# Kernel optimization log

Measured on AMD Instinct MI355X. Metric: run time of the kernel, lower is better.

Reference implementation:

```python
import jax, jax.numpy as jnp
import numpy as np

PC_RANGE = (-51.2, -51.2, -5.0, 51.2, 51.2, 3.0)
E, CAMS, LVLS = 256, 6, 4
LVL_HW = [(64, 176), (32, 88), (16, 44), (8, 22)]


def setup_inputs() -> dict:
    key = jax.random.key(0)
    ks = jax.random.split(key, 16)
    B, N = 2, 6400
    inp = {
        'instance_feature': jax.random.normal(ks[0], (B, N, E), jnp.float32),
        'anchor': jax.random.normal(ks[1], (B, N, 11), jnp.float32),
        'projection': jax.random.uniform(ks[2], (B, CAMS, 4, 4), jnp.float32),
    }
    for i, (H, W) in enumerate(LVL_HW):
        inp[f'feat{i}'] = jax.random.normal(ks[3 + i], (B, CAMS, E, H, W), jnp.float32)
    # learned params (random, not the zero-init of the module, to exercise the math)
    inp['attn_w'] = jax.random.normal(ks[8], (CAMS * LVLS, E), jnp.float32) * 0.02
    inp['attn_b'] = jax.random.normal(ks[9], (CAMS * LVLS,), jnp.float32) * 0.02
    inp['vp_w'] = jax.random.normal(ks[10], (E, E), jnp.float32) * (1.0 / np.sqrt(E))
    inp['vp_b'] = jnp.zeros((E,), jnp.float32)
    inp['op_w'] = jax.random.normal(ks[11], (E, E), jnp.float32) * (1.0 / np.sqrt(E))
    inp['op_b'] = jnp.zeros((E,), jnp.float32)
    return inp


def _bilinear_sample(feat, x, y):
    """feat: [BN, C, H, W]; x, y: [BN, N] pixel coords.
    Bilinear, zeros padding, align_corners=True (pixel coords == uv directly).
    Returns [BN, N, C]."""
    BN, C, H, W = feat.shape
    x0 = jnp.floor(x); y0 = jnp.floor(y)
    wx1 = x - x0; wx0 = 1.0 - wx1
    wy1 = y - y0; wy0 = 1.0 - wy1
    feat_flat = feat.reshape(BN, C, H * W)
    b = jnp.arange(BN)[:, None]

    def corner(xi, yi, w):
        valid = (xi >= 0) & (xi <= W - 1) & (yi >= 0) & (yi <= H - 1)
        xi_c = jnp.clip(xi, 0, W - 1).astype(jnp.int32)
        yi_c = jnp.clip(yi, 0, H - 1).astype(jnp.int32)
        idx = yi_c * W + xi_c                      # [BN, N]
        v = feat_flat[b, :, idx]                   # [BN, N, C]
        return v * (w * valid.astype(w.dtype))[..., None]

    return (corner(x0, y0, wx0 * wy0) + corner(x0 + 1, y0, wx1 * wy0)
            + corner(x0, y0 + 1, wx0 * wy1) + corner(x0 + 1, y0 + 1, wx1 * wy1))


def reference(instance_feature, anchor, projection, feat0, feat1, feat2, feat3,
              attn_w, attn_b, vp_w, vp_b, op_w, op_b):
    B, N, _ = instance_feature.shape
    feats = [feat0, feat1, feat2, feat3]
    # attention weights over cams x levels (softmax over levels, dim=-1)
    attn = (instance_feature @ attn_w.T + attn_b).reshape(B, N, CAMS, LVLS)
    attn = jax.nn.softmax(attn, axis=-1)
    # anchor center -> world coords
    xyz = jax.nn.sigmoid(anchor[..., :3])
    pr = jnp.asarray(PC_RANGE, dtype=anchor.dtype)
    xyz_world = xyz * (pr[3:6] - pr[0:3]) + pr[0:3]
    xyz_h = jnp.concatenate([xyz_world, jnp.ones((B, N, 1), anchor.dtype)], axis=-1)
    xyz_cam = jnp.einsum('bcij,bnj->bcni', projection, xyz_h)   # [B,CAMS,N,4]
    depth = jnp.maximum(xyz_cam[..., 2:3], 1e-4)
    uv = xyz_cam[..., :2] / depth                               # [B,CAMS,N,2] pixel coords
    BN = B * CAMS
    x = uv[..., 0].reshape(BN, N)
    y = uv[..., 1].reshape(BN, N)
    sampled = []
    for feat in feats:
        H, W = feat.shape[-2], feat.shape[-1]
        s = _bilinear_sample(feat.reshape(BN, E, H, W), x, y)   # [BN,N,E]
        sampled.append(s.reshape(B, CAMS, N, E))
    S = jnp.stack(sampled, axis=0)                              # [L,B,CAMS,N,E]
    out = jnp.einsum('lbcne,bncl->bne', S, attn)
    out = out @ vp_w.T + vp_b
    out = (out + instance_feature) @ op_w.T + op_b
    return out
```

## Files before the change

kernel.cpp:

```cpp
#include <hip/hip_runtime.h>
#include <hip/hip_fp16.h>
#include <math.h>

#define B_ 2
#define N_ 6400
#define E_ 256
#define C_ 6
#define L_ 4
#define SL2_ 128

__device__ __host__ constexpr int HWH[4] = {64, 32, 16, 8};
__device__ __host__ constexpr int HWW[4] = {176, 88, 44, 22};
__device__ __host__ constexpr int LOFF[4] = {0, 11264, 14080, 14784};
#define HWT 14960

struct __align__(8) H4 { __half2 lo, hi; };

typedef __attribute__((ext_vector_type(8))) _Float16 half8;
typedef __attribute__((ext_vector_type(4))) _Float16 half4;
typedef __attribute__((ext_vector_type(4))) float floatx4;

__global__ __launch_bounds__(256) void prep_kernel(
    const float* __restrict__ inst, const float* __restrict__ anchor,
    const float* __restrict__ proj, const float* __restrict__ attn_w,
    const float* __restrict__ attn_b,
    uint4* __restrict__ meta_w, int4* __restrict__ meta_b)
{
    __shared__ float AWT[256 * 24];
    __shared__ float ts[256 * 33];

    const int tid = threadIdx.x;

    for (int idx = tid; idx < 24 * 256; idx += 256) {
        int j = idx >> 8, k = idx & 255;
        AWT[k * 24 + j] = attn_w[idx];
    }
    __syncthreads();

    const int pt0 = blockIdx.x * 256;

    float acc[24];
#pragma unroll
    for (int j = 0; j < 24; j++) acc[j] = attn_b[j];

    for (int k0 = 0; k0 < 256; k0 += 32) {
#pragma unroll
        for (int r = 0; r < 32; r++) {
            int lin = r * 256 + tid;
            int p = lin >> 5, kk = lin & 31;
            ts[p * 33 + kk] = inst[(size_t)(pt0 + p) * 256 + k0 + kk];
        }
        __syncthreads();
#pragma unroll
        for (int kk = 0; kk < 32; kk++) {
            float v = ts[tid * 33 + kk];
            const float* aw = &AWT[(k0 + kk) * 24];
#pragma unroll
            for (int j = 0; j < 24; j++) acc[j] += v * aw[j];
        }
        __syncthreads();
    }

    const int pt = pt0 + tid;
    const int b = pt / N_;
    const int n = pt - b * N_;

    float attn[24];
#pragma unroll
    for (int c = 0; c < C_; c++) {
        float m = fmaxf(fmaxf(acc[c * 4], acc[c * 4 + 1]),
                        fmaxf(acc[c * 4 + 2], acc[c * 4 + 3]));
        float s = 0.f;
#pragma unroll
        for (int l = 0; l < L_; l++) {
            float e = expf(acc[c * 4 + l] - m);
            attn[c * 4 + l] = e;
            s += e;
        }
        float r = 1.f / s;
#pragma unroll
        for (int l = 0; l < L_; l++) attn[c * 4 + l] *= r;
    }

    float ax = anchor[(size_t)pt * 11 + 0];
    float ay = anchor[(size_t)pt * 11 + 1];
    float az = anchor[(size_t)pt * 11 + 2];
    float wxp = (1.f / (1.f + expf(-ax))) * 102.4f - 51.2f;
    float wyp = (1.f / (1.f + expf(-ay))) * 102.4f - 51.2f;
    float wzp = (1.f / (1.f + expf(-az))) * 8.f - 5.f;

#pragma unroll
    for (int c = 0; c < C_; c++) {
        const float* P = &proj[(size_t)(b * C_ + c) * 16];
        float cx = P[0] * wxp + P[1] * wyp + P[2] * wzp + P[3];
        float cy = P[4] * wxp + P[5] * wyp + P[6] * wzp + P[7];
        float cz = P[8] * wxp + P[9] * wyp + P[10] * wzp + P[11];
        float d = fmaxf(cz, 1e-4f);
        float u = cx / d, v = cy / d;

        float x0f = floorf(u), y0f = floorf(v);
        float fx1 = u - x0f, fy1 = v - y0f;
        float fx0 = 1.f - fx1, fy0 = 1.f - fy1;

        float4 wl[4]; int bsx[4];
#pragma unroll
        for (int l = 0; l < L_; l++) {
            const int W = HWW[l], H = HWH[l];
            float ax0, ax1; int bx;
            int ix = (int)fminf(fmaxf(x0f, -2.f), (float)W);
            if (ix <= -2 || ix >= W)      { ax0 = 0.f;  ax1 = 0.f;  bx = 0; }
            else if (ix == -1)            { ax0 = fx1;  ax1 = 0.f;  bx = 0; }
            else if (ix == W - 1)         { ax0 = 0.f;  ax1 = fx0;  bx = W - 2; }
            else                          { ax0 = fx0;  ax1 = fx1;  bx = ix; }
            float ay0, ay1; int by;
            int iy = (int)fminf(fmaxf(y0f, -2.f), (float)H);
            if (iy <= -2 || iy >= H)      { ay0 = 0.f;  ay1 = 0.f;  by = 0; }
            else if (iy == -1)            { ay0 = fy1;  ay1 = 0.f;  by = 0; }
            else if (iy == H - 1)         { ay0 = 0.f;  ay1 = fy0;  by = H - 2; }
            else                          { ay0 = fy0;  ay1 = fy1;  by = iy; }

            float a = attn[c * 4 + l];
            wl[l] = make_float4(a * ay0 * ax0, a * ay0 * ax1,
                                a * ay1 * ax0, a * ay1 * ax1);
            bsx[l] = by * W + bx;
        }
        size_t mi = (size_t)(b * C_ + c) * N_ + n;
        union { uint4 u; __half2 h[4]; } q0, q1;
        q0.h[0] = __floats2half2_rn(wl[0].x, wl[0].y);
        q0.h[1] = __floats2half2_rn(wl[0].z, wl[0].w);
        q0.h[2] = __floats2half2_rn(wl[1].x, wl[1].y);
        q0.h[3] = __floats2half2_rn(wl[1].z, wl[1].w);
        q1.h[0] = __floats2half2_rn(wl[2].x, wl[2].y);
        q1.h[1] = __floats2half2_rn(wl[2].z, wl[2].w);
        q1.h[2] = __floats2half2_rn(wl[3].x, wl[3].y);
        q1.h[3] = __floats2half2_rn(wl[3].z, wl[3].w);
        meta_w[mi * 2 + 0] = q0.u;
        meta_w[mi * 2 + 1] = q1.u;
        meta_b[mi] = make_int4(bsx[0], bsx[1], bsx[2], bsx[3]);
    }
}

template<bool PART>
__global__ __launch_bounds__(1024) void gather_t(
    const float* __restrict__ f0, const float* __restrict__ f1,
    const float* __restrict__ f2, const float* __restrict__ f3,
    const uint4* __restrict__ meta_w, const int4* __restrict__ meta_b,
    __half2* __restrict__ part2, float* __restrict__ agg)
{
    __shared__ __half2 lds2[HWT];

    const int tid = threadIdx.x;
    const int bid = blockIdx.x;
    const int slice = bid & 127;
    const int c = (bid >> 7) % C_;
    const int b = bid / (128 * C_);
    const int e0 = slice * 2;

    const float* fs[4] = {f0, f1, f2, f3};

#pragma unroll
    for (int l = 0; l < L_; l++) {
        const int HW = HWH[l] * HWW[l];
        const float* s0 = fs[l] + (size_t)((b * C_ + c) * E_ + e0) * HW;
        const float* s1 = s0 + HW;
        const int quarter = HW >> 2;
        for (int q = tid; q < quarter; q += 1024) {
            int p = q * 4;
            float4 v0 = *(const float4*)(s0 + p);
            float4 v1 = *(const float4*)(s1 + p);
            union { uint4 u; __half2 h[4]; } pk;
            pk.h[0] = __floats2half2_rn(v0.x, v1.x);
            pk.h[1] = __floats2half2_rn(v0.y, v1.y);
            pk.h[2] = __floats2half2_rn(v0.z, v1.z);
            pk.h[3] = __floats2half2_rn(v0.w, v1.w);
            *(uint4*)&lds2[LOFF[l] + p] = pk.u;
        }
    }
    __syncthreads();

    const size_t mbase = (size_t)(b * C_ + c) * N_;
    const uint4* mwp = meta_w + mbase * 2;
    const int4* mbp = meta_b + mbase;
    __half2* pout = part2 + ((size_t)(b * C_ + c) * SL2_ + slice) * N_;
    float* aggb = agg + (size_t)b * N_ * E_ + e0;

    int n = tid;
    uint4 m0, m1; int4 px;
    {
        m0 = mwp[(size_t)n * 2];
        m1 = mwp[(size_t)n * 2 + 1];
        px = mbp[n];
    }

    while (n < N_) {
        int nn = n + 1024;
        uint4 t0, t1; int4 px2;
        if (nn < N_) {
            t0 = mwp[(size_t)nn * 2];
            t1 = mwp[(size_t)nn * 2 + 1];
            px2 = mbp[nn];
        }

        union { uint4 u; __half2 h[4]; } a0u, a1u;
        a0u.u = m0; a1u.u = m1;
        float4 ws[4];
        {
            float2 p0 = __half22float2(a0u.h[0]), p1 = __half22float2(a0u.h[1]);
            float2 p2 = __half22float2(a0u.h[2]), p3 = __half22float2(a0u.h[3]);
            ws[0] = make_float4(p0.x, p0.y, p1.x, p1.y);
            ws[1] = make_float4(p2.x, p2.y, p3.x, p3.y);
            float2 p4 = __half22float2(a1u.h[0]), p5 = __half22float2(a1u.h[1]);
            float2 p6 = __half22float2(a1u.h[2]), p7 = __half22float2(a1u.h[3]);
            ws[2] = make_float4(p4.x, p4.y, p5.x, p5.y);
            ws[3] = make_float4(p6.x, p6.y, p7.x, p7.y);
        }
        const int pxs[4] = {px.x, px.y, px.z, px.w};

        float a0 = 0.f, a1 = 0.f;
#pragma unroll
        for (int l = 0; l < L_; l++) {
            float4 w = ws[l];
            if (w.x != 0.f || w.y != 0.f || w.z != 0.f || w.w != 0.f) {
                const int W = HWW[l];
                const int base = LOFF[l] + pxs[l];
                float2 f00 = __half22float2(lds2[base]);
                float2 f01 = __half22float2(lds2[base + 1]);
                float2 f10 = __half22float2(lds2[base + W]);
                float2 f11 = __half22float2(lds2[base + W + 1]);
                a0 += w.x * f00.x + w.y * f01.x + w.z * f10.x + w.w * f11.x;
                a1 += w.x * f00.y + w.y * f01.y + w.z * f10.y + w.w * f11.y;
            }
        }

        if (PART) {
            pout[n] = __floats2half2_rn(a0, a1);
        } else {
            if (a0 != 0.f || a1 != 0.f) {
                float* dst = aggb + (size_t)n * E_;
                atomicAdd(dst + 0, a0);
                atomicAdd(dst + 1, a1);
            }
        }

        n = nn;
        m0 = t0; m1 = t1; px = px2;
    }
}

#define SAS2 264
#define WSS2 72
#define KC 64

__global__ __launch_bounds__(256) void gemm_mfma(
    const float* __restrict__ inst,
    const float* __restrict__ vp_w, const float* __restrict__ vp_b,
    const float* __restrict__ op_w, const float* __restrict__ op_b,
    const __half2* __restrict__ part2, float* __restrict__ out)
{
    __shared__ _Float16 sA[32 * SAS2];
    __shared__ _Float16 sT[32 * SAS2];
    __shared__ _Float16 wS[256 * WSS2];

    const int tid = threadIdx.x;
    const int wave = tid >> 6;
    const int lane = tid & 63;
    const int mt = wave & 1;
    const int nh = wave >> 1;
    const int q = lane >> 4;
    const int col = lane & 15;

    const int p0 = blockIdx.x * 32;
    const int b = p0 / N_;
    const int nbase = p0 - b * N_;

    {
        const int p = tid & 31, sg = tid >> 5;
        const int n = nbase + p;
        for (int s = sg; s < SL2_; s += 8) {
            float a0 = 0.f, a1 = 0.f;
#pragma unroll
            for (int c = 0; c < C_; c++) {
                float2 f = __half22float2(
                    part2[((size_t)(b * C_ + c) * SL2_ + s) * N_ + n]);
                a0 += f.x; a1 += f.y;
            }
            sA[p * SAS2 + s * 2 + 0] = (_Float16)a0;
            sA[p * SAS2 + s * 2 + 1] = (_Float16)a1;
        }
    }

    floatx4 acc[8];
#pragma unroll
    for (int nt = 0; nt < 8; nt++) acc[nt] = (floatx4)(0.f);

    for (int kc = 0; kc < 256 / KC; kc++) {
        __syncthreads();
        {
            const float* src = vp_w + (size_t)tid * 256 + kc * KC;
            _Float16* dst = &wS[tid * WSS2];
#pragma unroll
            for (int i = 0; i < 8; i++) {
                float4 v = *(const float4*)(src + i * 8);
                float4 u = *(const float4*)(src + i * 8 + 4);
                half8 h = {(_Float16)v.x, (_Float16)v.y, (_Float16)v.z, (_Float16)v.w,
                           (_Float16)u.x, (_Float16)u.y, (_Float16)u.z, (_Float16)u.w};
                *(half8*)(dst + i * 8) = h;
            }
        }
        __syncthreads();
#pragma unroll
        for (int ks = 0; ks < KC / 32; ks++) {
            half8 a = *(half8*)&sA[(mt * 16 + col) * SAS2 + kc * KC + ks * 32 + q * 8];
#pragma unroll
            for (int nt = 0; nt < 8; nt++) {
                half8 bf = *(half8*)&wS[(nh * 128 + nt * 16 + col) * WSS2 + ks * 32 + q * 8];
                acc[nt] = __builtin_amdgcn_mfma_f32_16x16x32_f16(a, bf, acc[nt], 0, 0, 0);
            }
        }
    }

#pragma unroll
    for (int nt = 0; nt < 8; nt++) {
        const int e = nh * 128 + nt * 16 + col;
        const float bv = vp_b[e];
#pragma unroll
        for (int r = 0; r < 4; r++) {
            const int p = mt * 16 + q * 4 + r;
            float t = acc[nt][r] + bv + inst[(size_t)(p0 + p) * E_ + e];
            sT[p * SAS2 + e] = (_Float16)t;
        }
        acc[nt] = (floatx4)(0.f);
    }

    for (int kc = 0; kc < 256 / KC; kc++) {
        __syncthreads();
        {
            const float* src = op_w + (size_t)tid * 256 + kc * KC;
            _Float16* dst = &wS[tid * WSS2];
#pragma unroll
            for (int i = 0; i < 8; i++) {
                float4 v = *(const float4*)(src + i * 8);
                float4 u = *(const float4*)(src + i * 8 + 4);
                half8 h = {(_Float16)v.x, (_Float16)v.y, (_Float16)v.z, (_Float16)v.w,
                           (_Float16)u.x, (_Float16)u.y, (_Float16)u.z, (_Float16)u.w};
                *(half8*)(dst + i * 8) = h;
            }
        }
        __syncthreads();
#pragma unroll
        for (int ks = 0; ks < KC / 32; ks++) {
            half8 a = *(half8*)&sT[(mt * 16 + col) * SAS2 + kc * KC + ks * 32 + q * 8];
#pragma unroll
            for (int nt = 0; nt < 8; nt++) {
                half8 bf = *(half8*)&wS[(nh * 128 + nt * 16 + col) * WSS2 + ks * 32 + q * 8];
                acc[nt] = __builtin_amdgcn_mfma_f32_16x16x32_f16(a, bf, acc[nt], 0, 0, 0);
            }
        }
    }

#pragma unroll
    for (int nt = 0; nt < 8; nt++) {
        const int e = nh * 128 + nt * 16 + col;
        const float ob = op_b[e];
#pragma unroll
        for (int r = 0; r < 4; r++) {
            const int p = mt * 16 + q * 4 + r;
            out[(size_t)(p0 + p) * E_ + e] = acc[nt][r] + ob;
        }
    }
}

#define PT 32
#define SAS 264
#define WSS 36

__global__ __launch_bounds__(256) void gemm_valu(
    const float* __restrict__ inst,
    const float* __restrict__ vp_w, const float* __restrict__ vp_b,
    const float* __restrict__ op_w, const float* __restrict__ op_b,
    float* __restrict__ io)
{
    __shared__ __align__(16) float sA[PT * SAS];
    __shared__ __align__(16) float wS[256 * WSS];

    const int tid = threadIdx.x;
    const int eg = tid & 31;
    const int pg = tid >> 5;
    const int p0 = blockIdx.x * PT;

#pragma unroll
    for (int r = 0; r < PT; r++)
        sA[r * SAS + tid] = io[(size_t)(p0 + r) * E_ + tid];
    __syncthreads();

    float acc[4][8];
#pragma unroll
    for (int j = 0; j < 4; j++)
#pragma unroll
        for (int i = 0; i < 8; i++) acc[j][i] = 0.f;

    for (int k0 = 0; k0 < 256; k0 += 32) {
        __syncthreads();
#pragma unroll
        for (int r = 0; r < 32; r++) {
            int lin = r * 256 + tid;
            int e = lin >> 5, kk = lin & 31;
            wS[e * WSS + kk] = vp_w[(size_t)e * 256 + k0 + kk];
        }
        __syncthreads();
#pragma unroll
        for (int kk = 0; kk < 32; kk += 4) {
            float4 wv4[8], av4[4];
#pragma unroll
            for (int i = 0; i < 8; i++)
                wv4[i] = *(const float4*)&wS[(eg + 32 * i) * WSS + kk];
#pragma unroll
            for (int j = 0; j < 4; j++)
                av4[j] = *(const float4*)&sA[(pg * 4 + j) * SAS + k0 + kk];
#pragma unroll
            for (int j = 0; j < 4; j++)
#pragma unroll
                for (int i = 0; i < 8; i++)
                    acc[j][i] += av4[j].x * wv4[i].x + av4[j].y * wv4[i].y
                               + av4[j].z * wv4[i].z + av4[j].w * wv4[i].w;
        }
    }

    __syncthreads();
#pragma unroll
    for (int j = 0; j < 4; j++) {
        int p = pg * 4 + j;
#pragma unroll
        for (int i = 0; i < 8; i++) {
            int e = eg + 32 * i;
            float t = acc[j][i] + vp_b[e] + inst[(size_t)(p0 + p) * E_ + e];
            sA[p * SAS + e] = t;
            acc[j][i] = 0.f;
        }
    }

    for (int k0 = 0; k0 < 256; k0 += 32) {
        __syncthreads();
#pragma unroll
        for (int r = 0; r < 32; r++) {
            int lin = r * 256 + tid;
            int e = lin >> 5, kk = lin & 31;
            wS[e * WSS + kk] = op_w[(size_t)e * 256 + k0 + kk];
        }
        __syncthreads();
#pragma unroll
        for (int kk = 0; kk < 32; kk += 4) {
            float4 wv4[8], av4[4];
#pragma unroll
            for (int i = 0; i < 8; i++)
                wv4[i] = *(const float4*)&wS[(eg + 32 * i) * WSS + kk];
#pragma unroll
            for (int j = 0; j < 4; j++)
                av4[j] = *(const float4*)&sA[(pg * 4 + j) * SAS + k0 + kk];
#pragma unroll
            for (int j = 0; j < 4; j++)
#pragma unroll
                for (int i = 0; i < 8; i++)
                    acc[j][i] += av4[j].x * wv4[i].x + av4[j].y * wv4[i].y
                               + av4[j].z * wv4[i].z + av4[j].w * wv4[i].w;
        }
    }

#pragma unroll
    for (int j = 0; j < 4; j++) {
        int p = pg * 4 + j;
#pragma unroll
        for (int i = 0; i < 8; i++) {
            int e = eg + 32 * i;
            io[(size_t)(p0 + p) * E_ + e] = acc[j][i] + op_b[e];
        }
    }
}

extern "C" void kernel_launch(void* const* d_in, const int* in_sizes, int n_in,
                              void* d_out, int out_size, void* d_ws, size_t ws_size,
                              hipStream_t stream)
{
    const float* inst   = (const float*)d_in[0];
    const float* anchor = (const float*)d_in[1];
    const float* proj   = (const float*)d_in[2];
    const float* f0     = (const float*)d_in[3];
    const float* f1     = (const float*)d_in[4];
    const float* f2     = (const float*)d_in[5];
    const float* f3     = (const float*)d_in[6];
    const float* attn_w = (const float*)d_in[7];
    const float* attn_b = (const float*)d_in[8];
    const float* vp_w   = (const float*)d_in[9];
    const float* vp_b   = (const float*)d_in[10];
    const float* op_w   = (const float*)d_in[11];
    const float* op_b   = (const float*)d_in[12];
    float* out = (float*)d_out;

    const size_t NPT = (size_t)B_ * C_ * N_;
    uint4* meta_w = (uint4*)d_ws;
    int4* meta_b = (int4*)((char*)d_ws + NPT * 32);
    __half2* part2 = (__half2*)((char*)d_ws + NPT * 48);
    const size_t need = NPT * 48 + (size_t)B_ * C_ * SL2_ * N_ * sizeof(__half2);

    prep_kernel<<<(B_ * N_) / 256, 256, 0, stream>>>(
        inst, anchor, proj, attn_w, attn_b, meta_w, meta_b);

    if (ws_size >= need) {
        gather_t<true><<<B_ * C_ * SL2_, 1024, 0, stream>>>(
            f0, f1, f2, f3, meta_w, meta_b, part2, out);
        gemm_mfma<<<(B_ * N_) / 32, 256, 0, stream>>>(
            inst, vp_w, vp_b, op_w, op_b, part2, out);
    } else {
        hipMemsetAsync(d_out, 0, (size_t)out_size * sizeof(float), stream);
        gather_t<false><<<B_ * C_ * SL2_, 1024, 0, stream>>>(
            f0, f1, f2, f3, meta_w, meta_b, part2, out);
        gemm_valu<<<(B_ * N_) / PT, 256, 0, stream>>>(
            inst, vp_w, vp_b, op_w, op_b, out);
    }
}
```

Baseline: 354.4 us.

## Compact visible sample points per camera before gathering to skip invisible ones

Adds a stream-compaction kernel that, for each batch-camera segment, keeps only the sample points with nonzero bilinear weights and writes their metadata into a dense list along with the original index. A new gather kernel zero-fills its output slice, stages the features in LDS, and then runs only over the compacted list, scattering each result to its original position. The aim is to stop spending LDS reads and arithmetic on points that project outside the image. In exchange it adds an extra kernel launch, a serial per-segment scan in only 12 blocks, zero-fill writes, and needs a larger workspace.

```diff
diff --git a/kernel.cpp b/kernel.cpp
--- a/kernel.cpp
+++ b/kernel.cpp
@@ -137,6 +137,162 @@
         meta_w[mi * 2 + 0] = q0.u;
         meta_w[mi * 2 + 1] = q1.u;
         meta_b[mi] = make_int4(bsx[0], bsx[1], bsx[2], bsx[3]);
+    }
+}
+
+__global__ __launch_bounds__(1024) void compact_kernel(
+    const uint4* __restrict__ meta_w, const int4* __restrict__ meta_b,
+    uint4* __restrict__ cmeta_w, int4* __restrict__ cmeta_b,
+    int* __restrict__ counts)
+{
+    const int seg = blockIdx.x;
+    const size_t base = (size_t)seg * N_;
+    __shared__ int wsum[17];
+
+    const int tid = threadIdx.x;
+    const int lane = tid & 63;
+    const int wv = tid >> 6;
+
+    int running = 0;
+    for (int c0 = 0; c0 < N_; c0 += 1024) {
+        const int n = c0 + tid;
+        const bool valid = n < N_;
+        uint4 m0 = make_uint4(0, 0, 0, 0), m1 = make_uint4(0, 0, 0, 0);
+        int4 bx = make_int4(0, 0, 0, 0);
+        if (valid) {
+            m0 = meta_w[(base + n) * 2];
+            m1 = meta_w[(base + n) * 2 + 1];
+            bx = meta_b[base + n];
+        }
+        const bool vis = valid &&
+            ((m0.x | m0.y | m0.z | m0.w | m1.x | m1.y | m1.z | m1.w) != 0u);
+
+        unsigned long long ball = __ballot(vis);
+        int wpre = __popcll(ball & ((1ull << lane) - 1ull));
+        if (lane == 0) wsum[wv] = __popcll(ball);
+        __syncthreads();
+        if (tid == 0) {
+            int r = 0;
+#pragma unroll
+            for (int w = 0; w < 16; w++) { int t = wsum[w]; wsum[w] = r; r += t; }
+            wsum[16] = r;
+        }
+        __syncthreads();
+        const int pos = running + wsum[wv] + wpre;
+        const int ctot = wsum[16];
+
+        if (vis) {
+            cmeta_w[(base + pos) * 2]     = m0;
+            cmeta_w[(base + pos) * 2 + 1] = m1;
+            cmeta_b[base + pos] = make_int4(bx.x | (bx.y << 16),
+                                            bx.z | (bx.w << 16), n, 0);
+        }
+        running += ctot;
+        __syncthreads();
+    }
+    if (tid == 0) counts[seg] = running;
+}
+
+__global__ __launch_bounds__(1024) void gather_compact(
+    const float* __restrict__ f0, const float* __restrict__ f1,
+    const float* __restrict__ f2, const float* __restrict__ f3,
+    const uint4* __restrict__ cmeta_w, const int4* __restrict__ cmeta_b,
+    const int* __restrict__ counts, __half2* __restrict__ part2)
+{
+    __shared__ __half2 lds2[HWT];
+
+    const int tid = threadIdx.x;
+    const int bid = blockIdx.x;
+    const int slice = bid & 127;
+    const int c = (bid >> 7) % C_;
+    const int b = bid / (128 * C_);
+    const int e0 = slice * 2;
+    const int bc = b * C_ + c;
+
+    __half2* pout = part2 + ((size_t)bc * SL2_ + slice) * N_;
+
+    for (int z = tid; z < 1600; z += 1024)
+        ((uint4*)pout)[z] = make_uint4(0, 0, 0, 0);
+
+    const float* fs[4] = {f0, f1, f2, f3};
+
+#pragma unroll
+    for (int l = 0; l < L_; l++) {
+        const int HW = HWH[l] * HWW[l];
+        const float* s0 = fs[l] + (size_t)(bc * E_ + e0) * HW;
+        const float* s1 = s0 + HW;
+        const int quarter = HW >> 2;
+        for (int q = tid; q < quarter; q += 1024) {
+            int p = q * 4;
+            float4 v0 = *(const float4*)(s0 + p);
+            float4 v1 = *(const float4*)(s1 + p);
+            union { uint4 u; __half2 h[4]; } pk;
+            pk.h[0] = __floats2half2_rn(v0.x, v1.x);
+            pk.h[1] = __floats2half2_rn(v0.y, v1.y);
+            pk.h[2] = __floats2half2_rn(v0.z, v1.z);
+            pk.h[3] = __floats2half2_rn(v0.w, v1.w);
+            *(uint4*)&lds2[LOFF[l] + p] = pk.u;
+        }
+    }
+    __syncthreads();
+
+    const int nvis = counts[bc];
+    const uint4* mwp = cmeta_w + (size_t)bc * N_ * 2;
+    const int4* mbp = cmeta_b + (size_t)bc * N_;
+
+    int i = tid;
+    uint4 m0, m1; int4 cb;
+    if (i < nvis) {
+        m0 = mwp[(size_t)i * 2];
+        m1 = mwp[(size_t)i * 2 + 1];
+        cb = mbp[i];
+    }
+
+    while (i < nvis) {
+        int ii = i + 1024;
+        uint4 t0, t1; int4 tb;
+        if (ii < nvis) {
+            t0 = mwp[(size_t)ii * 2];
+            t1 = mwp[(size_t)ii * 2 + 1];
+            tb = mbp[ii];
+        }
+
+        union { uint4 u; __half2 h[4]; } a0u, a1u;
+        a0u.u = m0; a1u.u = m1;
+        __half2 wh[8];
+        wh[0] = a0u.h[0]; wh[1] = a0u.h[1]; wh[2] = a0u.h[2]; wh[3] = a0u.h[3];
+        wh[4] = a1u.h[0]; wh[5] = a1u.h[1]; wh[6] = a1u.h[2]; wh[7] = a1u.h[3];
+
+        int bs[4];
+        bs[0] = cb.x & 0xffff;
+        bs[1] = ((unsigned)cb.x) >> 16;
+        bs[2] = cb.y & 0xffff;
+        bs[3] = ((unsigned)cb.y) >> 16;
+        const int outn = cb.z;
+
+        float p0[4], p1[4];
+#pragma unroll
+        for (int l = 0; l < L_; l++) {
+            const int W = HWW[l];
+            const int base = LOFF[l] + bs[l];
+            float2 wab = __half22float2(wh[l * 2]);
+            float2 wcd = __half22float2(wh[l * 2 + 1]);
+            float2 f00 = __half22float2(lds2[base]);
+            float2 f01 = __half22float2(lds2[base + 1]);
+            float2 f10 = __half22float2(lds2[base + W]);
+            float2 f11 = __half22float2(lds2[base + W + 1]);
+            p0[l] = (wab.x * f00.x + wab.y * f01.x)
+                  + (wcd.x * f10.x + wcd.y * f11.x);
+            p1[l] = (wab.x * f00.y + wab.y * f01.y)
+                  + (wcd.x * f10.y + wcd.y * f11.y);
+        }
+        float a0 = (p0[0] + p0[1]) + (p0[2] + p0[3]);
+        float a1 = (p1[0] + p1[1]) + (p1[2] + p1[3]);
+
+        pout[outn] = __floats2half2_rn(a0, a1);
+
+        i = ii;
+        m0 = t0; m1 = t1; cb = tb;
     }
 }
 
@@ -500,12 +656,24 @@
     uint4* meta_w = (uint4*)d_ws;
     int4* meta_b = (int4*)((char*)d_ws + NPT * 32);
     __half2* part2 = (__half2*)((char*)d_ws + NPT * 48);
-    const size_t need = NPT * 48 + (size_t)B_ * C_ * SL2_ * N_ * sizeof(__half2);
+    const size_t part2_bytes = (size_t)B_ * C_ * SL2_ * N_ * sizeof(__half2);
+    const size_t need = NPT * 48 + part2_bytes;
+    uint4* cmeta_w = (uint4*)((char*)d_ws + need);
+    int4* cmeta_b = (int4*)((char*)d_ws + need + NPT * 32);
+    int* counts = (int*)((char*)d_ws + need + NPT * 48);
+    const size_t need_cmp = need + NPT * 48 + 256;
 
     prep_kernel<<<(B_ * N_) / 256, 256, 0, stream>>>(
         inst, anchor, proj, attn_w, attn_b, meta_w, meta_b);
 
-    if (ws_size >= need) {
+    if (ws_size >= need_cmp) {
+        compact_kernel<<<B_ * C_, 1024, 0, stream>>>(
+            meta_w, meta_b, cmeta_w, cmeta_b, counts);
+        gather_compact<<<B_ * C_ * SL2_, 1024, 0, stream>>>(
+            f0, f1, f2, f3, cmeta_w, cmeta_b, counts, part2);
+        gemm_mfma<<<(B_ * N_) / 32, 256, 0, stream>>>(
+            inst, vp_w, vp_b, op_w, op_b, part2, out);
+    } else if (ws_size >= need) {
         gather_t<true><<<B_ * C_ * SL2_, 1024, 0, stream>>>(
             f0, f1, f2, f3, meta_w, meta_b, part2, out);
         gemm_mfma<<<(B_ * N_) / 32, 256, 0, stream>>>(
```

Measured after the change: 362.7 us. +2.4%, slower.

## Swizzle gather block order, deepen metadata prefetch, and double GEMM row tile

Applied to the files above, without the earlier changes.

The gather kernel now remaps block IDs so consecutive blocks (by (bid&7)*192+(bid>>3)) work on different (batch, camera) pairs, which likely spreads feature and metadata traffic across the chip. Its metadata loads are prefetched two iterations ahead instead of one, to hide global load latency. The fused projection GEMM now processes 64 rows per block with 512 threads and 8 waves, and splits the weight staging across two threads per row, so each converted weight chunk is reused by twice as many rows. The cost is more LDS and register pressure per block and fewer GEMM blocks in flight.

```diff
diff --git a/kernel.cpp b/kernel.cpp
--- a/kernel.cpp
+++ b/kernel.cpp
@@ -14,10 +14,7 @@
 __device__ __host__ constexpr int LOFF[4] = {0, 11264, 14080, 14784};
 #define HWT 14960
 
-struct __align__(8) H4 { __half2 lo, hi; };
-
 typedef __attribute__((ext_vector_type(8))) _Float16 half8;
-typedef __attribute__((ext_vector_type(4))) _Float16 half4;
 typedef __attribute__((ext_vector_type(4))) float floatx4;
 
 __global__ __launch_bounds__(256) void prep_kernel(
@@ -150,18 +147,20 @@
     __shared__ __half2 lds2[HWT];
 
     const int tid = threadIdx.x;
-    const int bid = blockIdx.x;
+    int bid = blockIdx.x;
+    bid = (bid & 7) * 192 + (bid >> 3);
     const int slice = bid & 127;
     const int c = (bid >> 7) % C_;
     const int b = bid / (128 * C_);
     const int e0 = slice * 2;
+    const int bc = b * C_ + c;
 
     const float* fs[4] = {f0, f1, f2, f3};
 
 #pragma unroll
     for (int l = 0; l < L_; l++) {
         const int HW = HWH[l] * HWW[l];
-        const float* s0 = fs[l] + (size_t)((b * C_ + c) * E_ + e0) * HW;
+        const float* s0 = fs[l] + (size_t)(bc * E_ + e0) * HW;
         const float* s1 = s0 + HW;
         const int quarter = HW >> 2;
         for (int q = tid; q < quarter; q += 1024) {
@@ -178,27 +177,33 @@
     }
     __syncthreads();
 
-    const size_t mbase = (size_t)(b * C_ + c) * N_;
+    const size_t mbase = (size_t)bc * N_;
     const uint4* mwp = meta_w + mbase * 2;
     const int4* mbp = meta_b + mbase;
-    __half2* pout = part2 + ((size_t)(b * C_ + c) * SL2_ + slice) * N_;
+    __half2* pout = part2 + ((size_t)bc * SL2_ + slice) * N_;
     float* aggb = agg + (size_t)b * N_ * E_ + e0;
 
     int n = tid;
     uint4 m0, m1; int4 px;
+    uint4 o0, o1; int4 ox;
     {
         m0 = mwp[(size_t)n * 2];
         m1 = mwp[(size_t)n * 2 + 1];
         px = mbp[n];
     }
+    if (n + 1024 < N_) {
+        o0 = mwp[(size_t)(n + 1024) * 2];
+        o1 = mwp[(size_t)(n + 1024) * 2 + 1];
+        ox = mbp[n + 1024];
+    }
 
     while (n < N_) {
-        int nn = n + 1024;
-        uint4 t0, t1; int4 px2;
-        if (nn < N_) {
-            t0 = mwp[(size_t)nn * 2];
-            t1 = mwp[(size_t)nn * 2 + 1];
-            px2 = mbp[nn];
+        const int n2 = n + 2048;
+        uint4 t0, t1; int4 tx;
+        if (n2 < N_) {
+            t0 = mwp[(size_t)n2 * 2];
+            t1 = mwp[(size_t)n2 * 2 + 1];
+            tx = mbp[n2];
         }
 
         union { uint4 u; __half2 h[4]; } a0u, a1u;
@@ -242,8 +247,9 @@
             }
         }
 
-        n = nn;
-        m0 = t0; m1 = t1; px = px2;
+        n += 1024;
+        m0 = o0; m1 = o1; px = ox;
+        o0 = t0; o1 = t1; ox = tx;
     }
 }
 
@@ -251,30 +257,30 @@
 #define WSS2 72
 #define KC 64
 
-__global__ __launch_bounds__(256) void gemm_mfma(
+__global__ __launch_bounds__(512) void gemm_mfma(
     const float* __restrict__ inst,
     const float* __restrict__ vp_w, const float* __restrict__ vp_b,
     const float* __restrict__ op_w, const float* __restrict__ op_b,
     const __half2* __restrict__ part2, float* __restrict__ out)
 {
-    __shared__ _Float16 sA[32 * SAS2];
-    __shared__ _Float16 sT[32 * SAS2];
+    __shared__ _Float16 sA[64 * SAS2];
+    __shared__ _Float16 sT[64 * SAS2];
     __shared__ _Float16 wS[256 * WSS2];
 
     const int tid = threadIdx.x;
     const int wave = tid >> 6;
     const int lane = tid & 63;
-    const int mt = wave & 1;
-    const int nh = wave >> 1;
+    const int mt = wave & 3;
+    const int nh = wave >> 2;
     const int q = lane >> 4;
     const int col = lane & 15;
 
-    const int p0 = blockIdx.x * 32;
+    const int p0 = blockIdx.x * 64;
     const int b = p0 / N_;
     const int nbase = p0 - b * N_;
 
     {
-        const int p = tid & 31, sg = tid >> 5;
+        const int p = tid & 63, sg = tid >> 6;
         const int n = nbase + p;
         for (int s = sg; s < SL2_; s += 8) {
             float a0 = 0.f, a1 = 0.f;
@@ -296,10 +302,11 @@
     for (int kc = 0; kc < 256 / KC; kc++) {
         __syncthreads();
         {
-            const float* src = vp_w + (size_t)tid * 256 + kc * KC;
-            _Float16* dst = &wS[tid * WSS2];
-#pragma unroll
-            for (int i = 0; i < 8; i++) {
+            const int row = tid >> 1, half = tid & 1;
+            const float* src = vp_w + (size_t)row * 256 + kc * KC + half * 32;
+            _Float16* dst = &wS[row * WSS2 + half * 32];
+#pragma unroll
+            for (int i = 0; i < 4; i++) {
                 float4 v = *(const float4*)(src + i * 8);
                 float4 u = *(const float4*)(src + i * 8 + 4);
                 half8 h = {(_Float16)v.x, (_Float16)v.y, (_Float16)v.z, (_Float16)v.w,
@@ -335,10 +342,11 @@
     for (int kc = 0; kc < 256 / KC; kc++) {
         __syncthreads();
         {
-            const float* src = op_w + (size_t)tid * 256 + kc * KC;
-            _Float16* dst = &wS[tid * WSS2];
-#pragma unroll
-            for (int i = 0; i < 8; i++) {
+            const int row = tid >> 1, half = tid & 1;
+            const float* src = op_w + (size_t)row * 256 + kc * KC + half * 32;
+            _Float16* dst = &wS[row * WSS2 + half * 32];
+#pragma unroll
+            for (int i = 0; i < 4; i++) {
                 float4 v = *(const float4*)(src + i * 8);
                 float4 u = *(const float4*)(src + i * 8 + 4);
                 half8 h = {(_Float16)v.x, (_Float16)v.y, (_Float16)v.z, (_Float16)v.w,
@@ -500,7 +508,8 @@
     uint4* meta_w = (uint4*)d_ws;
     int4* meta_b = (int4*)((char*)d_ws + NPT * 32);
     __half2* part2 = (__half2*)((char*)d_ws + NPT * 48);
-    const size_t need = NPT * 48 + (size_t)B_ * C_ * SL2_ * N_ * sizeof(__half2);
+    const size_t part2_bytes = (size_t)B_ * C_ * SL2_ * N_ * sizeof(__half2);
+    const size_t need = NPT * 48 + part2_bytes;
 
     prep_kernel<<<(B_ * N_) / 256, 256, 0, stream>>>(
         inst, anchor, proj, attn_w, attn_b, meta_w, meta_b);
@@ -508,7 +517,7 @@
     if (ws_size >= need) {
         gather_t<true><<<B_ * C_ * SL2_, 1024, 0, stream>>>(
             f0, f1, f2, f3, meta_w, meta_b, part2, out);
-        gemm_mfma<<<(B_ * N_) / 32, 256, 0, stream>>>(
+        gemm_mfma<<<(B_ * N_) / 64, 512, 0, stream>>>(
             inst, vp_w, vp_b, op_w, op_b, part2, out);
     } else {
         hipMemsetAsync(d_out, 0, (size_t)out_size * sizeof(float), stream);
```

New measurement: 348.8 us. Within noise of the previous version (-1.6%).
